# Kernel optimization log

Hardware: AMD Instinct MI355X
Metric: run time of the kernel (lower is better)

Reference implementation:

```python
import jax, jax.numpy as jnp
import numpy as np

HD = 8   # hidden_dim per node
H = 28
W = 28
B = 16


def conv2d(x, w, b):
    y = jax.lax.conv_general_dilated(x, w, (1, 1), 'SAME',
                                     dimension_numbers=('NCHW', 'OIHW', 'NCHW'))
    return y + b[None, :, None, None]


def gru_cell(x, h, td, gw, gb, cw, cb):
    # ConvGRU cell with multiplicative topdown modulation of the gate input.
    combined = jnp.concatenate([x, h], axis=1) * jax.nn.sigmoid(td)  # (B,2HD,H,W)
    r, u = jnp.split(jax.nn.sigmoid(conv2d(combined, gw, gb)), 2, axis=1)
    cand = jnp.tanh(conv2d(jnp.concatenate([x, r * h], axis=1), cw, cb))
    return (1.0 - u) * h + u * cand


def td_proj(td, w, b):
    # dynamic nn.Linear: (B, HD*H*W) -> (B, 2*HD*H*W), reshaped to feature map
    out = td.reshape(td.shape[0], -1) @ w.T + b
    return out.reshape(td.shape[0], 2 * HD, H, W)


def setup_inputs():
    key = jax.random.key(0)
    ks = jax.random.split(key, 16)
    s = 0.02
    return {
        'input_tensor': jax.random.normal(ks[0], (B, 3, 1, H, W), jnp.float32),
        'topdown_input': jax.random.normal(ks[1], (B, 2 * HD, H, W), jnp.float32),
        'input_conv_w': jax.random.normal(ks[2], (HD, 3, 3, 3), jnp.float32) * s,
        'input_conv_b': jnp.zeros((HD,), jnp.float32),
        'gates_w': jax.random.normal(ks[3], (3, 2 * HD, 2 * HD, 3, 3), jnp.float32) * s,
        'gates_b': jnp.zeros((3, 2 * HD), jnp.float32),
        'can_w': jax.random.normal(ks[4], (3, HD, 2 * HD, 3, 3), jnp.float32) * s,
        'can_b': jnp.zeros((3, HD), jnp.float32),
        'td_w0': jax.random.normal(ks[5], (2 * HD * H * W, HD * H * W), jnp.float32) * s,
        'td_b0': jnp.zeros((2 * HD * H * W,), jnp.float32),
        'td_w1': jax.random.normal(ks[6], (2 * HD * H * W, HD * H * W), jnp.float32) * s,
        'td_b1': jnp.zeros((2 * HD * H * W,), jnp.float32),
        'fc1_w': jax.random.normal(ks[7], (100, HD * H * W), jnp.float32) * s,
        'fc1_b': jnp.zeros((100,), jnp.float32),
        'fc2_w': jax.random.normal(ks[8], (10, 100), jnp.float32) * s,
        'fc2_b': jnp.zeros((10,), jnp.float32),
    }


def reference(input_tensor, topdown_input, input_conv_w, input_conv_b,
              gates_w, gates_b, can_w, can_b,
              td_w0, td_b0, td_w1, td_b1, fc1_w, fc1_b, fc2_w, fc2_b):
    b = input_tensor.shape[0]
    z = jnp.zeros((b, HD, H, W), input_tensor.dtype)
    prev = [z, z, z]
    cur = [z, z, z]
    # input layout (b,c,t,h,w); permute+index picks frame t=0
    cur_input = conv2d(input_tensor[:, :, 0], input_conv_w, input_conv_b)
    for step in range(2):  # reps=2, max(seq_len, max_rank)=1 -> 2 graph sweeps
        # node 0 (input node): bottomup = input conv; feedback from node 1 (0.6)
        td0 = td_proj(0.6 * prev[1], td_w0, td_b0)
        cur[0] = gru_cell(cur_input, prev[0], td0,
                          gates_w[0], gates_b[0], can_w[0], can_b[0])
        # node 1: feedforward from node 0 (0.8); feedback from node 2 (0.5)
        td1 = td_proj(0.5 * prev[2], td_w1, td_b1)
        cur[1] = gru_cell(0.8 * prev[0], prev[1], td1,
                          gates_w[1], gates_b[1], can_w[1], can_b[1])
        # node 2 (output node): feedforward from node 1 (0.7); external topdown
        cur[2] = gru_cell(0.7 * prev[1], prev[2], topdown_input,
                          gates_w[2], gates_b[2], can_w[2], can_b[2])
        # faithful to torch: hidden_state_prev = hidden_state_cur aliases the
        # list, so sweeps after the first see in-sweep node updates
        prev = cur
    pred = jax.nn.relu(cur[2].reshape(b, -1)) @ fc1_w.T + fc1_b
    pred = jax.nn.relu(pred) @ fc2_w.T + fc2_b
    return pred
```

## Files before the change

kernel.cpp:

```cpp
#include <hip/hip_runtime.h>
#include <cstddef>

#define HD 8
#define C2 16
#define HH 28
#define WW 28
#define BB 16
#define SP (HH*WW)
#define FEAT (HD*SP)
#define FEAT2 (C2*SP)

#define TILE_ROWS 2
#define NT (HH/TILE_ROWS)
#define NBLK (BB*NT)
#define NTHR 512

#define X0_R 18
#define H00_R 14
#define H10_R 10
#define H11_R 6

__device__ __forceinline__ float sigf(float x) { return 1.0f / (1.0f + expf(-x)); }

union F4 { float4 v; float f[4]; };

struct SM {
    float gwt[C2*9][16];
    float cwt[C2*9][8];
    float gb[C2];
    float cb[HD];
    float hc1[HD];
    float hc2[HD];
    float comb[C2][18][32];
    union {
        float rh[HD][16][32];
        float s_in[3][TILE_ROWS+18][32];
    } u;
    float su[HD][14][32];
    float x0e[HD][X0_R][32];
    float h00e[HD][H00_R][32];
    float h10e[HD][H10_R][32];
    float h11e[HD][H11_R][32];
};

__device__ __forceinline__ void gbar(unsigned* arrive, unsigned* release,
                                     int blk, unsigned ep) {
    __syncthreads();
    __threadfence();
    if (threadIdx.x == 0)
        __hip_atomic_store(&arrive[(size_t)blk * 16], ep,
                           __ATOMIC_RELEASE, __HIP_MEMORY_SCOPE_AGENT);
    if (blk == 0) {
        int t = threadIdx.x;
        if (t < NBLK) {
            while (__hip_atomic_load(&arrive[(size_t)t * 16],
                                     __ATOMIC_RELAXED, __HIP_MEMORY_SCOPE_AGENT) < ep)
                __builtin_amdgcn_s_sleep(32);
        }
        __syncthreads();
        if (t < NBLK)
            __hip_atomic_store(&release[(size_t)t * 16], ep,
                               __ATOMIC_RELEASE, __HIP_MEMORY_SCOPE_AGENT);
    } else {
        if (threadIdx.x == 0) {
            while (__hip_atomic_load(&release[(size_t)blk * 16],
                                     __ATOMIC_RELAXED, __HIP_MEMORY_SCOPE_AGENT) < ep)
                __builtin_amdgcn_s_sleep(32);
        }
    }
    __threadfence();
    __syncthreads();
}

__device__ __forceinline__ void stage_node(SM& sm, int tid, int n,
                           const float* gates_w, const float* gates_b,
                           const float* can_w, const float* can_b) {
    for (int i = tid; i < C2*C2*9; i += NTHR) {
        int oc = i & 15, r = i >> 4;
        sm.gwt[r][oc] = gates_w[n*C2*C2*9 + oc*C2*9 + r];
    }
    for (int i = tid; i < C2*9*8; i += NTHR) {
        int oc = i & 7, r = i >> 3;
        sm.cwt[r][oc] = can_w[n*HD*C2*9 + oc*C2*9 + r];
    }
    if (tid < C2) sm.gb[tid] = gates_b[n*C2 + tid];
    if (tid < HD) sm.cb[tid] = can_b[n*HD + tid];
}

template<int XS>
__device__ __forceinline__ const float* xrow(SM& sm, int c, int ridx) {
    if constexpr (XS == 0) return &sm.x0e[c][ridx][0];
    else if constexpr (XS == 1) return &sm.h10e[c][ridx][0];
    else return &sm.h11e[c][ridx][0];
}

template<int M, int XS, int HS, int OS>
__device__ void cell(SM& sm, int tid, int bi, int r0, float xs,
                     const float* __restrict__ td, float* __restrict__ h12g) {
    constexpr int R1 = M + 4, R2 = M + 2;
    constexpr int NIC = (HS == 0) ? HD : C2;
    const int ca    = (OS == 0) ? r0-6 : (OS == 1) ? r0-4 : (OS == 2) ? r0-2 : r0;
    const int xbase = (XS == 0) ? r0-8 : (XS == 1) ? r0-4 : r0-2;
    const int hbase = r0 - 6;

    for (int i = tid; i < NIC*R1*8; i += NTHR) {
        int ci4 = i & 7, rr = (i >> 3) % R1, c = i / (8*R1);
        int row = ca - 2 + rr;
        F4 v; v.f[0] = v.f[1] = v.f[2] = v.f[3] = 0.0f;
        if (row >= 0 && row < HH) {
            F4 base;
            if (c < HD) {
                base.v = *(const float4*)(xrow<XS>(sm, c, row - xbase) + ci4*4);
                #pragma unroll
                for (int e = 0; e < 4; ++e) base.f[e] *= xs;
            } else {
                if constexpr (HS == 1)
                    base.v = *(const float4*)(&sm.h00e[c-HD][row - hbase][ci4*4]);
                else if constexpr (HS == 2) {
                    float h = sm.hc1[c-HD];
                    base.f[0] = base.f[1] = base.f[2] = base.f[3] = h;
                } else {
                    float h = sm.hc2[c-HD];
                    base.f[0] = base.f[1] = base.f[2] = base.f[3] = h;
                }
            }
            const float* tdr = td + c*SP + row*WW;
            #pragma unroll
            for (int e = 0; e < 4; ++e) {
                int col = ci4*4 + e - 2;
                if (col >= 0 && col < WW)
                    v.f[e] = base.f[e] * sigf(tdr[col]);
            }
        }
        *(float4*)&sm.comb[c][rr][ci4*4] = v.v;
    }
    __syncthreads();

    constexpr int itemsU = 2*M*32;
    if constexpr (HS != 0) {
        constexpr int itemsB = 2*R2*32;
        for (int i = tid; i < itemsB + itemsU; i += NTHR) {
            if (i < itemsB) {
                int ci = i & 31, rr = (i >> 5) % R2, g = i / (32*R2);
                int row = ca - 1 + rr, col = ci - 2;
                bool inb = (col >= 0 && col < WW && row >= 0 && row < HH);
                float a0 = sm.gb[g*4+0], a1 = sm.gb[g*4+1],
                      a2 = sm.gb[g*4+2], a3 = sm.gb[g*4+3];
                if (inb) {
                    #pragma unroll 2
                    for (int ic = 0; ic < C2; ++ic) {
                        const float* wb = &sm.gwt[ic*9][g*4];
                        #pragma unroll
                        for (int dy = 0; dy < 3; ++dy)
                            #pragma unroll
                            for (int dx = 0; dx < 3; ++dx) {
                                float cvv = sm.comb[ic][rr+dy][ci-1+dx];
                                F4 w; w.v = *(const float4*)(wb + (dy*3+dx)*16);
                                a0 += cvv*w.f[0]; a1 += cvv*w.f[1];
                                a2 += cvv*w.f[2]; a3 += cvv*w.f[3];
                            }
                    }
                }
                float av[4] = {a0, a1, a2, a3};
                #pragma unroll
                for (int o = 0; o < 4; ++o) {
                    int c = g*4 + o;
                    float v = 0.0f;
                    if (inb) {
                        float hv;
                        if constexpr (HS == 1) hv = sm.h00e[c][row - hbase][ci];
                        else if constexpr (HS == 2) hv = sm.hc1[c];
                        else hv = sm.hc2[c];
                        v = sigf(av[o]) * hv;
                    }
                    sm.u.rh[c][rr][ci] = v;
                }
            } else {
                int j = i - itemsB;
                int ci = j & 31, rr = (j >> 5) % M, g = j / (32*M);
                int row = ca + rr, col = ci - 2;
                bool inb = (col >= 0 && col < WW && row >= 0 && row < HH);
                float a0 = sm.gb[HD+g*4+0], a1 = sm.gb[HD+g*4+1],
                      a2 = sm.gb[HD+g*4+2], a3 = sm.gb[HD+g*4+3];
                if (inb) {
                    #pragma unroll 2
                    for (int ic = 0; ic < C2; ++ic) {
                        const float* wb = &sm.gwt[ic*9][HD + g*4];
                        #pragma unroll
                        for (int dy = 0; dy < 3; ++dy)
                            #pragma unroll
                            for (int dx = 0; dx < 3; ++dx) {
                                float cvv = sm.comb[ic][rr+1+dy][ci-1+dx];
                                F4 w; w.v = *(const float4*)(wb + (dy*3+dx)*16);
                                a0 += cvv*w.f[0]; a1 += cvv*w.f[1];
                                a2 += cvv*w.f[2]; a3 += cvv*w.f[3];
                            }
                    }
                }
                float av[4] = {a0, a1, a2, a3};
                #pragma unroll
                for (int o = 0; o < 4; ++o)
                    sm.su[g*4+o][rr][ci] = sigf(av[o]);
            }
        }
    } else {
        for (int i = tid; i < itemsU; i += NTHR) {
            int ci = i & 31, rr = (i >> 5) % M, g = i / (32*M);
            int row = ca + rr, col = ci - 2;
            bool inb = (col >= 0 && col < WW && row >= 0 && row < HH);
            float a0 = sm.gb[HD+g*4+0], a1 = sm.gb[HD+g*4+1],
                  a2 = sm.gb[HD+g*4+2], a3 = sm.gb[HD+g*4+3];
            if (inb) {
                #pragma unroll 2
                for (int ic = 0; ic < HD; ++ic) {
                    const float* wb = &sm.gwt[ic*9][HD + g*4];
                    #pragma unroll
                    for (int dy = 0; dy < 3; ++dy)
                        #pragma unroll
                        for (int dx = 0; dx < 3; ++dx) {
                            float cvv = sm.comb[ic][rr+1+dy][ci-1+dx];
                            F4 w; w.v = *(const float4*)(wb + (dy*3+dx)*16);
                            a0 += cvv*w.f[0]; a1 += cvv*w.f[1];
                            a2 += cvv*w.f[2]; a3 += cvv*w.f[3];
                        }
                }
            }
            float av[4] = {a0, a1, a2, a3};
            #pragma unroll
            for (int o = 0; o < 4; ++o)
                sm.su[g*4+o][rr][ci] = sigf(av[o]);
        }
    }
    __syncthreads();

    for (int i = tid; i < 2*M*32; i += NTHR) {
        int ci = i & 31, rr = (i >> 5) % M, g = i / (32*M);
        int row = ca + rr, col = ci - 2;
        bool inb = (col >= 0 && col < WW && row >= 0 && row < HH);
        float a0 = sm.cb[g*4+0], a1 = sm.cb[g*4+1],
              a2 = sm.cb[g*4+2], a3 = sm.cb[g*4+3];
        if (inb) {
            #pragma unroll 2
            for (int ic = 0; ic < HD; ++ic) {
                const float* wb = &sm.cwt[ic*9][g*4];
                #pragma unroll
                for (int dy = 0; dy < 3; ++dy) {
                    const float* xr = xrow<XS>(sm, ic, (row - 1 + dy) - xbase);
                    #pragma unroll
                    for (int dx = 0; dx < 3; ++dx) {
                        float civ = xs * xr[ci-1+dx];
                        F4 w; w.v = *(const float4*)(wb + (dy*3+dx)*8);
                        a0 += civ*w.f[0]; a1 += civ*w.f[1];
                        a2 += civ*w.f[2]; a3 += civ*w.f[3];
                    }
                }
            }
            if constexpr (HS != 0) {
                #pragma unroll 2
                for (int ic = HD; ic < C2; ++ic) {
                    const float* wb = &sm.cwt[ic*9][g*4];
                    #pragma unroll
                    for (int dy = 0; dy < 3; ++dy)
                        #pragma unroll
                        for (int dx = 0; dx < 3; ++dx) {
                            float civ = sm.u.rh[ic-HD][rr+dy][ci-1+dx];
                            F4 w; w.v = *(const float4*)(wb + (dy*3+dx)*8);
                            a0 += civ*w.f[0]; a1 += civ*w.f[1];
                            a2 += civ*w.f[2]; a3 += civ*w.f[3];
                        }
                }
            }
        }
        float av[4] = {a0, a1, a2, a3};
        #pragma unroll
        for (int o = 0; o < 4; ++o) {
            int c = g*4 + o;
            float outv = 0.0f;
            if (inb) {
                float uu = sm.su[c][rr][ci];
                float cand = tanhf(av[o]);
                float hv;
                if constexpr (HS == 1) hv = sm.h00e[c][row - hbase][ci];
                else if constexpr (HS == 2) hv = sm.hc1[c];
                else if constexpr (HS == 3) hv = sm.hc2[c];
                else hv = 0.0f;
                outv = (1.0f - uu) * hv + uu * cand;
            }
            if constexpr (OS == 0) sm.h00e[c][row - (r0-6)][ci] = outv;
            else if constexpr (OS == 1) sm.h10e[c][row - (r0-4)][ci] = outv;
            else if constexpr (OS == 2) sm.h11e[c][row - (r0-2)][ci] = outv;
            else {
                if (inb)
                    h12g[((size_t)bi*HD + c)*SP + row*WW + col] = outv;
            }
        }
    }
    __syncthreads();
}

__global__ void init_kernel(unsigned* arrive, unsigned* release) {
    int t = threadIdx.x;
    for (int i = t; i < NBLK*16; i += 256) { arrive[i] = 0u; release[i] = 0u; }
}

__global__ __launch_bounds__(NTHR, 2)
void mega_kernel(const float* __restrict__ input_tensor, const float* __restrict__ topdown,
                 const float* __restrict__ icw, const float* __restrict__ icb,
                 const float* __restrict__ gates_w, const float* __restrict__ gates_b,
                 const float* __restrict__ can_w, const float* __restrict__ can_b,
                 const float* __restrict__ td_w0, const float* __restrict__ td_b0,
                 const float* __restrict__ td_w1, const float* __restrict__ td_b1,
                 float* __restrict__ h12g,
                 float* __restrict__ td0c, float* __restrict__ td1c,
                 unsigned* arrive, unsigned* release)
{
    const int tid = threadIdx.x;
    const int blk = blockIdx.x;
    const int bi  = blk / NT;
    const int r0  = (blk % NT) * TILE_ROWS;

    __shared__ SM sm;

    if (tid < HD) {
        sm.hc1[tid] = sigf(gates_b[1*C2 + HD + tid]) * tanhf(can_b[1*HD + tid]);
        sm.hc2[tid] = sigf(gates_b[2*C2 + HD + tid]) * tanhf(can_b[2*HD + tid]);
    }
    bool f0 = false, f1 = false;
    for (int c = 0; c < HD; ++c) {
        f0 |= (sigf(gates_b[1*C2 + HD + c]) * tanhf(can_b[1*HD + c])) != 0.0f;
        f1 |= (sigf(gates_b[2*C2 + HD + c]) * tanhf(can_b[2*HD + c])) != 0.0f;
    }

    for (int i = tid; i < 3*(TILE_ROWS+18)*32; i += NTHR) {
        int ci = i & 31, rr = (i >> 5) % (TILE_ROWS+18), c = i / (32*(TILE_ROWS+18));
        int row = r0 - 9 + rr, col = ci - 2;
        float v = 0.0f;
        if (row >= 0 && row < HH && col >= 0 && col < WW)
            v = input_tensor[((size_t)bi*3 + c)*SP + row*WW + col];
        sm.u.s_in[c][rr][ci] = v;
    }
    for (int i = tid; i < 3*9*8; i += NTHR) {
        int oc = i & 7, r = i >> 3;
        sm.gwt[r][oc] = icw[oc*27 + r];
    }
    if (tid < HD) sm.cb[tid] = icb[tid];
    __syncthreads();

    for (int i = tid; i < X0_R*32; i += NTHR) {
        int ci = i & 31, rr = i >> 5;
        int row = r0 - 8 + rr, col = ci - 2;
        float acc[8];
        if (row >= 0 && row < HH && col >= 0 && col < WW) {
            #pragma unroll
            for (int o = 0; o < 8; ++o) acc[o] = sm.cb[o];
            for (int ic = 0; ic < 3; ++ic)
                #pragma unroll
                for (int dy = 0; dy < 3; ++dy)
                    #pragma unroll
                    for (int dx = 0; dx < 3; ++dx) {
                        float a = sm.u.s_in[ic][rr+dy][ci-1+dx];
                        F4 w0, w1;
                        w0.v = *(const float4*)&sm.gwt[ic*9+dy*3+dx][0];
                        w1.v = *(const float4*)&sm.gwt[ic*9+dy*3+dx][4];
                        acc[0] += a*w0.f[0]; acc[1] += a*w0.f[1];
                        acc[2] += a*w0.f[2]; acc[3] += a*w0.f[3];
                        acc[4] += a*w1.f[0]; acc[5] += a*w1.f[1];
                        acc[6] += a*w1.f[2]; acc[7] += a*w1.f[3];
                    }
        } else {
            #pragma unroll
            for (int o = 0; o < 8; ++o) acc[o] = 0.0f;
        }
        #pragma unroll
        for (int o = 0; o < 8; ++o) sm.x0e[o][rr][ci] = acc[o];
    }
    __syncthreads();

    stage_node(sm, tid, 0, gates_w, gates_b, can_w, can_b);
    cell<14, 0, 0, 0>(sm, tid, bi, r0, 1.0f, td_b0, nullptr);

    if (f0 | f1) {
        if (f0) {
            for (int j = blk*NTHR + tid; j < FEAT2; j += NBLK*NTHR) {
                float s = td_b0[j];
                const float* wr = td_w0 + (size_t)j * FEAT;
                for (int c = 0; c < HD; ++c) {
                    float hcv = sm.hc1[c];
                    if (hcv != 0.0f) {
                        float ss = 0.0f;
                        for (int p = 0; p < SP; ++p) ss += wr[c*SP + p];
                        s += 0.6f * hcv * ss;
                    }
                }
                td0c[j] = s;
            }
        }
        if (f1) {
            for (int j = blk*NTHR + tid; j < FEAT2; j += NBLK*NTHR) {
                float s = td_b1[j];
                const float* wr = td_w1 + (size_t)j * FEAT;
                for (int c = 0; c < HD; ++c) {
                    float hcv = sm.hc2[c];
                    if (hcv != 0.0f) {
                        float ss = 0.0f;
                        for (int p = 0; p < SP; ++p) ss += wr[c*SP + p];
                        s += 0.5f * hcv * ss;
                    }
                }
                td1c[j] = s;
            }
        }
        gbar(arrive, release, blk, 1u);
    }
    const float* td0v = f0 ? td0c : td_b0;
    const float* td1v = f1 ? td1c : td_b1;

    cell<10, 0, 1, 1>(sm, tid, bi, r0, 1.0f, td0v, nullptr);

    stage_node(sm, tid, 1, gates_w, gates_b, can_w, can_b);
    cell<6, 1, 2, 2>(sm, tid, bi, r0, 0.8f, td1v, nullptr);

    stage_node(sm, tid, 2, gates_w, gates_b, can_w, can_b);
    cell<2, 2, 3, 3>(sm, tid, bi, r0, 0.7f, topdown + (size_t)bi*FEAT2, h12g);
}

__global__ __launch_bounds__(256)
void fc1_kernel(const float* __restrict__ in, const float* __restrict__ w,
                const float* __restrict__ b, float* __restrict__ out) {
    int j    = blockIdx.x;
    int wave = threadIdx.x >> 6;
    int lane = threadIdx.x & 63;
    float acc[4] = {0.f, 0.f, 0.f, 0.f};
    const float* wr = w + (size_t)j * FEAT;
    for (int k = lane; k < FEAT; k += 64) {
        float wv = wr[k];
        #pragma unroll
        for (int q = 0; q < 4; ++q) {
            float v = in[(size_t)(wave*4+q)*FEAT + k];
            acc[q] += fmaxf(v, 0.0f) * wv;
        }
    }
    #pragma unroll
    for (int off = 32; off > 0; off >>= 1)
        #pragma unroll
        for (int q = 0; q < 4; ++q)
            acc[q] += __shfl_down(acc[q], off);
    if (lane == 0) {
        #pragma unroll
        for (int q = 0; q < 4; ++q)
            out[(size_t)(wave*4+q)*100 + j] = acc[q] + b[j];
    }
}

__global__ __launch_bounds__(256)
void fc2_kernel(const float* __restrict__ p1, const float* __restrict__ w,
                const float* __restrict__ b, float* __restrict__ out) {
    int t = threadIdx.x;
    if (t >= BB*10) return;
    int bi = t / 10, j = t % 10;
    float acc = b[j];
    for (int k = 0; k < 100; ++k)
        acc += fmaxf(p1[bi*100 + k], 0.0f) * w[j*100 + k];
    out[bi*10 + j] = acc;
}

extern "C" void kernel_launch(void* const* d_in, const int* in_sizes, int n_in,
                              void* d_out, int out_size, void* d_ws, size_t ws_size,
                              hipStream_t stream) {
    const float* input_tensor = (const float*)d_in[0];
    const float* topdown      = (const float*)d_in[1];
    const float* icw  = (const float*)d_in[2];
    const float* icb  = (const float*)d_in[3];
    const float* gates_w = (const float*)d_in[4];
    const float* gates_b = (const float*)d_in[5];
    const float* can_w   = (const float*)d_in[6];
    const float* can_b   = (const float*)d_in[7];
    const float* td_w0 = (const float*)d_in[8];
    const float* td_b0 = (const float*)d_in[9];
    const float* td_w1 = (const float*)d_in[10];
    const float* td_b1 = (const float*)d_in[11];
    const float* fc1_w = (const float*)d_in[12];
    const float* fc1_b = (const float*)d_in[13];
    const float* fc2_w = (const float*)d_in[14];
    const float* fc2_b = (const float*)d_in[15];
    float* out = (float*)d_out;

    float* ws   = (float*)d_ws;
    float* h12g = ws;
    float* p1   = h12g + BB*HD*SP;
    float* td0c = p1 + BB*100;
    float* td1c = td0c + FEAT2;
    unsigned* arrive  = (unsigned*)((char*)d_ws + (16u << 20));
    unsigned* release = arrive + NBLK*16;

    init_kernel<<<1, 256, 0, stream>>>(arrive, release);
    mega_kernel<<<NBLK, NTHR, 0, stream>>>(
        input_tensor, topdown, icw, icb, gates_w, gates_b, can_w, can_b,
        td_w0, td_b0, td_w1, td_b1,
        h12g, td0c, td1c, arrive, release);
    fc1_kernel<<<100, 256, 0, stream>>>(h12g, fc1_w, fc1_b, p1);
    fc2_kernel<<<1, 256, 0, stream>>>(p1, fc2_w, fc2_b, out);
}
```

Before: 111.5 us.

## Fuse fc1/fc2 into mega kernel via grid barriers and keep update gate in registers

The fc1 and fc2 layers, which ran as separate kernels, now run at the tail of the persistent mega kernel, separated by two extra grid-wide barriers. This removes two kernel launches and their launch gaps. The update-gate sigmoids are now held in per-thread registers instead of a shared-memory array, which frees LDS and drops one store/load pass, at the cost of extra register pressure and less interleaving of the reset and update convolutions. The spin-wait sleep interval is also halved to cut barrier wake-up latency.

```diff
diff --git a/kernel.cpp b/kernel.cpp
--- a/kernel.cpp
+++ b/kernel.cpp
@@ -36,7 +36,6 @@
         float rh[HD][16][32];
         float s_in[3][TILE_ROWS+18][32];
     } u;
-    float su[HD][14][32];
     float x0e[HD][X0_R][32];
     float h00e[HD][H00_R][32];
     float h10e[HD][H10_R][32];
@@ -55,7 +54,7 @@
         if (t < NBLK) {
             while (__hip_atomic_load(&arrive[(size_t)t * 16],
                                      __ATOMIC_RELAXED, __HIP_MEMORY_SCOPE_AGENT) < ep)
-                __builtin_amdgcn_s_sleep(32);
+                __builtin_amdgcn_s_sleep(16);
         }
         __syncthreads();
         if (t < NBLK)
@@ -65,7 +64,7 @@
         if (threadIdx.x == 0) {
             while (__hip_atomic_load(&release[(size_t)blk * 16],
                                      __ATOMIC_RELAXED, __HIP_MEMORY_SCOPE_AGENT) < ep)
-                __builtin_amdgcn_s_sleep(32);
+                __builtin_amdgcn_s_sleep(16);
         }
     }
     __threadfence();
@@ -99,6 +98,7 @@
                      const float* __restrict__ td, float* __restrict__ h12g) {
     constexpr int R1 = M + 4, R2 = M + 2;
     constexpr int NIC = (HS == 0) ? HD : C2;
+    constexpr int ITER_U = (2*M*32 + NTHR - 1) / NTHR;
     const int ca    = (OS == 0) ? r0-6 : (OS == 1) ? r0-4 : (OS == 2) ? r0-2 : r0;
     const int xbase = (XS == 0) ? r0-8 : (XS == 1) ? r0-4 : r0-2;
     const int hbase = r0 - 6;
@@ -136,75 +136,50 @@
     }
     __syncthreads();
 
-    constexpr int itemsU = 2*M*32;
     if constexpr (HS != 0) {
-        constexpr int itemsB = 2*R2*32;
-        for (int i = tid; i < itemsB + itemsU; i += NTHR) {
-            if (i < itemsB) {
-                int ci = i & 31, rr = (i >> 5) % R2, g = i / (32*R2);
-                int row = ca - 1 + rr, col = ci - 2;
-                bool inb = (col >= 0 && col < WW && row >= 0 && row < HH);
-                float a0 = sm.gb[g*4+0], a1 = sm.gb[g*4+1],
-                      a2 = sm.gb[g*4+2], a3 = sm.gb[g*4+3];
+        for (int i = tid; i < 2*R2*32; i += NTHR) {
+            int ci = i & 31, rr = (i >> 5) % R2, g = i / (32*R2);
+            int row = ca - 1 + rr, col = ci - 2;
+            bool inb = (col >= 0 && col < WW && row >= 0 && row < HH);
+            float a0 = sm.gb[g*4+0], a1 = sm.gb[g*4+1],
+                  a2 = sm.gb[g*4+2], a3 = sm.gb[g*4+3];
+            if (inb) {
+                #pragma unroll 2
+                for (int ic = 0; ic < C2; ++ic) {
+                    const float* wb = &sm.gwt[ic*9][g*4];
+                    #pragma unroll
+                    for (int dy = 0; dy < 3; ++dy)
+                        #pragma unroll
+                        for (int dx = 0; dx < 3; ++dx) {
+                            float cvv = sm.comb[ic][rr+dy][ci-1+dx];
+                            F4 w; w.v = *(const float4*)(wb + (dy*3+dx)*16);
+                            a0 += cvv*w.f[0]; a1 += cvv*w.f[1];
+                            a2 += cvv*w.f[2]; a3 += cvv*w.f[3];
+                        }
+                }
+            }
+            float av[4] = {a0, a1, a2, a3};
+            #pragma unroll
+            for (int o = 0; o < 4; ++o) {
+                int c = g*4 + o;
+                float v = 0.0f;
                 if (inb) {
-                    #pragma unroll 2
-                    for (int ic = 0; ic < C2; ++ic) {
-                        const float* wb = &sm.gwt[ic*9][g*4];
-                        #pragma unroll
-                        for (int dy = 0; dy < 3; ++dy)
-                            #pragma unroll
-                            for (int dx = 0; dx < 3; ++dx) {
-                                float cvv = sm.comb[ic][rr+dy][ci-1+dx];
-                                F4 w; w.v = *(const float4*)(wb + (dy*3+dx)*16);
-                                a0 += cvv*w.f[0]; a1 += cvv*w.f[1];
-                                a2 += cvv*w.f[2]; a3 += cvv*w.f[3];
-                            }
-                    }
-                }
-                float av[4] = {a0, a1, a2, a3};
-                #pragma unroll
-                for (int o = 0; o < 4; ++o) {
-                    int c = g*4 + o;
-                    float v = 0.0f;
-                    if (inb) {
-                        float hv;
-                        if constexpr (HS == 1) hv = sm.h00e[c][row - hbase][ci];
-                        else if constexpr (HS == 2) hv = sm.hc1[c];
-                        else hv = sm.hc2[c];
-                        v = sigf(av[o]) * hv;
-                    }
-                    sm.u.rh[c][rr][ci] = v;
-                }
-            } else {
-                int j = i - itemsB;
-                int ci = j & 31, rr = (j >> 5) % M, g = j / (32*M);
-                int row = ca + rr, col = ci - 2;
-                bool inb = (col >= 0 && col < WW && row >= 0 && row < HH);
-                float a0 = sm.gb[HD+g*4+0], a1 = sm.gb[HD+g*4+1],
-                      a2 = sm.gb[HD+g*4+2], a3 = sm.gb[HD+g*4+3];
-                if (inb) {
-                    #pragma unroll 2
-                    for (int ic = 0; ic < C2; ++ic) {
-                        const float* wb = &sm.gwt[ic*9][HD + g*4];
-                        #pragma unroll
-                        for (int dy = 0; dy < 3; ++dy)
-                            #pragma unroll
-                            for (int dx = 0; dx < 3; ++dx) {
-                                float cvv = sm.comb[ic][rr+1+dy][ci-1+dx];
-                                F4 w; w.v = *(const float4*)(wb + (dy*3+dx)*16);
-                                a0 += cvv*w.f[0]; a1 += cvv*w.f[1];
-                                a2 += cvv*w.f[2]; a3 += cvv*w.f[3];
-                            }
-                    }
-                }
-                float av[4] = {a0, a1, a2, a3};
-                #pragma unroll
-                for (int o = 0; o < 4; ++o)
-                    sm.su[g*4+o][rr][ci] = sigf(av[o]);
-            }
-        }
-    } else {
-        for (int i = tid; i < itemsU; i += NTHR) {
+                    float hv;
+                    if constexpr (HS == 1) hv = sm.h00e[c][row - hbase][ci];
+                    else if constexpr (HS == 2) hv = sm.hc1[c];
+                    else hv = sm.hc2[c];
+                    v = sigf(av[o]) * hv;
+                }
+                sm.u.rh[c][rr][ci] = v;
+            }
+        }
+    }
+
+    float su_reg[ITER_U][4];
+    #pragma unroll
+    for (int k = 0; k < ITER_U; ++k) {
+        int i = tid + k*NTHR;
+        if (i < 2*M*32) {
             int ci = i & 31, rr = (i >> 5) % M, g = i / (32*M);
             int row = ca + rr, col = ci - 2;
             bool inb = (col >= 0 && col < WW && row >= 0 && row < HH);
@@ -212,7 +187,7 @@
                   a2 = sm.gb[HD+g*4+2], a3 = sm.gb[HD+g*4+3];
             if (inb) {
                 #pragma unroll 2
-                for (int ic = 0; ic < HD; ++ic) {
+                for (int ic = 0; ic < NIC; ++ic) {
                     const float* wb = &sm.gwt[ic*9][HD + g*4];
                     #pragma unroll
                     for (int dy = 0; dy < 3; ++dy)
@@ -225,73 +200,75 @@
                         }
                 }
             }
-            float av[4] = {a0, a1, a2, a3};
-            #pragma unroll
-            for (int o = 0; o < 4; ++o)
-                sm.su[g*4+o][rr][ci] = sigf(av[o]);
-        }
-    }
-    __syncthreads();
-
-    for (int i = tid; i < 2*M*32; i += NTHR) {
-        int ci = i & 31, rr = (i >> 5) % M, g = i / (32*M);
-        int row = ca + rr, col = ci - 2;
-        bool inb = (col >= 0 && col < WW && row >= 0 && row < HH);
-        float a0 = sm.cb[g*4+0], a1 = sm.cb[g*4+1],
-              a2 = sm.cb[g*4+2], a3 = sm.cb[g*4+3];
-        if (inb) {
-            #pragma unroll 2
-            for (int ic = 0; ic < HD; ++ic) {
-                const float* wb = &sm.cwt[ic*9][g*4];
-                #pragma unroll
-                for (int dy = 0; dy < 3; ++dy) {
-                    const float* xr = xrow<XS>(sm, ic, (row - 1 + dy) - xbase);
-                    #pragma unroll
-                    for (int dx = 0; dx < 3; ++dx) {
-                        float civ = xs * xr[ci-1+dx];
-                        F4 w; w.v = *(const float4*)(wb + (dy*3+dx)*8);
-                        a0 += civ*w.f[0]; a1 += civ*w.f[1];
-                        a2 += civ*w.f[2]; a3 += civ*w.f[3];
-                    }
-                }
-            }
-            if constexpr (HS != 0) {
+            su_reg[k][0] = sigf(a0); su_reg[k][1] = sigf(a1);
+            su_reg[k][2] = sigf(a2); su_reg[k][3] = sigf(a3);
+        }
+    }
+    __syncthreads();
+
+    #pragma unroll
+    for (int k = 0; k < ITER_U; ++k) {
+        int i = tid + k*NTHR;
+        if (i < 2*M*32) {
+            int ci = i & 31, rr = (i >> 5) % M, g = i / (32*M);
+            int row = ca + rr, col = ci - 2;
+            bool inb = (col >= 0 && col < WW && row >= 0 && row < HH);
+            float a0 = sm.cb[g*4+0], a1 = sm.cb[g*4+1],
+                  a2 = sm.cb[g*4+2], a3 = sm.cb[g*4+3];
+            if (inb) {
                 #pragma unroll 2
-                for (int ic = HD; ic < C2; ++ic) {
+                for (int ic = 0; ic < HD; ++ic) {
                     const float* wb = &sm.cwt[ic*9][g*4];
                     #pragma unroll
-                    for (int dy = 0; dy < 3; ++dy)
+                    for (int dy = 0; dy < 3; ++dy) {
+                        const float* xr = xrow<XS>(sm, ic, (row - 1 + dy) - xbase);
                         #pragma unroll
                         for (int dx = 0; dx < 3; ++dx) {
-                            float civ = sm.u.rh[ic-HD][rr+dy][ci-1+dx];
+                            float civ = xs * xr[ci-1+dx];
                             F4 w; w.v = *(const float4*)(wb + (dy*3+dx)*8);
                             a0 += civ*w.f[0]; a1 += civ*w.f[1];
                             a2 += civ*w.f[2]; a3 += civ*w.f[3];
                         }
-                }
-            }
-        }
-        float av[4] = {a0, a1, a2, a3};
-        #pragma unroll
-        for (int o = 0; o < 4; ++o) {
-            int c = g*4 + o;
-            float outv = 0.0f;
-            if (inb) {
-                float uu = sm.su[c][rr][ci];
-                float cand = tanhf(av[o]);
-                float hv;
-                if constexpr (HS == 1) hv = sm.h00e[c][row - hbase][ci];
-                else if constexpr (HS == 2) hv = sm.hc1[c];
-                else if constexpr (HS == 3) hv = sm.hc2[c];
-                else hv = 0.0f;
-                outv = (1.0f - uu) * hv + uu * cand;
-            }
-            if constexpr (OS == 0) sm.h00e[c][row - (r0-6)][ci] = outv;
-            else if constexpr (OS == 1) sm.h10e[c][row - (r0-4)][ci] = outv;
-            else if constexpr (OS == 2) sm.h11e[c][row - (r0-2)][ci] = outv;
-            else {
-                if (inb)
-                    h12g[((size_t)bi*HD + c)*SP + row*WW + col] = outv;
+                    }
+                }
+                if constexpr (HS != 0) {
+                    #pragma unroll 2
+                    for (int ic = HD; ic < C2; ++ic) {
+                        const float* wb = &sm.cwt[ic*9][g*4];
+                        #pragma unroll
+                        for (int dy = 0; dy < 3; ++dy)
+                            #pragma unroll
+                            for (int dx = 0; dx < 3; ++dx) {
+                                float civ = sm.u.rh[ic-HD][rr+dy][ci-1+dx];
+                                F4 w; w.v = *(const float4*)(wb + (dy*3+dx)*8);
+                                a0 += civ*w.f[0]; a1 += civ*w.f[1];
+                                a2 += civ*w.f[2]; a3 += civ*w.f[3];
+                            }
+                    }
+                }
+            }
+            float av[4] = {a0, a1, a2, a3};
+            #pragma unroll
+            for (int o = 0; o < 4; ++o) {
+                int c = g*4 + o;
+                float outv = 0.0f;
+                if (inb) {
+                    float uu = su_reg[k][o];
+                    float cand = tanhf(av[o]);
+                    float hv;
+                    if constexpr (HS == 1) hv = sm.h00e[c][row - hbase][ci];
+                    else if constexpr (HS == 2) hv = sm.hc1[c];
+                    else if constexpr (HS == 3) hv = sm.hc2[c];
+                    else hv = 0.0f;
+                    outv = (1.0f - uu) * hv + uu * cand;
+                }
+                if constexpr (OS == 0) sm.h00e[c][row - (r0-6)][ci] = outv;
+                else if constexpr (OS == 1) sm.h10e[c][row - (r0-4)][ci] = outv;
+                else if constexpr (OS == 2) sm.h11e[c][row - (r0-2)][ci] = outv;
+                else {
+                    if (inb)
+                        h12g[((size_t)bi*HD + c)*SP + row*WW + col] = outv;
+                }
             }
         }
     }
@@ -310,7 +287,10 @@
                  const float* __restrict__ can_w, const float* __restrict__ can_b,
                  const float* __restrict__ td_w0, const float* __restrict__ td_b0,
                  const float* __restrict__ td_w1, const float* __restrict__ td_b1,
-                 float* __restrict__ h12g,
+                 const float* __restrict__ fc1_w, const float* __restrict__ fc1_b,
+                 const float* __restrict__ fc2_w, const float* __restrict__ fc2_b,
+                 float* __restrict__ out,
+                 float* __restrict__ h12g, float* __restrict__ p1,
                  float* __restrict__ td0c, float* __restrict__ td1c,
                  unsigned* arrive, unsigned* release)
 {
@@ -320,6 +300,7 @@
     const int r0  = (blk % NT) * TILE_ROWS;
 
     __shared__ SM sm;
+    unsigned ep = 0;
 
     if (tid < HD) {
         sm.hc1[tid] = sigf(gates_b[1*C2 + HD + tid]) * tanhf(can_b[1*HD + tid]);
@@ -410,7 +391,7 @@
                 td1c[j] = s;
             }
         }
-        gbar(arrive, release, blk, 1u);
+        gbar(arrive, release, blk, ++ep);
     }
     const float* td0v = f0 ? td0c : td_b0;
     const float* td1v = f1 ? td1c : td_b1;
@@ -422,46 +403,42 @@
 
     stage_node(sm, tid, 2, gates_w, gates_b, can_w, can_b);
     cell<2, 2, 3, 3>(sm, tid, bi, r0, 0.7f, topdown + (size_t)bi*FEAT2, h12g);
-}
-
-__global__ __launch_bounds__(256)
-void fc1_kernel(const float* __restrict__ in, const float* __restrict__ w,
-                const float* __restrict__ b, float* __restrict__ out) {
-    int j    = blockIdx.x;
-    int wave = threadIdx.x >> 6;
-    int lane = threadIdx.x & 63;
-    float acc[4] = {0.f, 0.f, 0.f, 0.f};
-    const float* wr = w + (size_t)j * FEAT;
-    for (int k = lane; k < FEAT; k += 64) {
-        float wv = wr[k];
+
+    gbar(arrive, release, blk, ++ep);
+    if (blk < 100 && tid < 256) {
+        int j    = blk;
+        int wave = tid >> 6;
+        int lane = tid & 63;
+        float acc[4] = {0.f, 0.f, 0.f, 0.f};
+        const float* wr = fc1_w + (size_t)j * FEAT;
+        for (int k = lane; k < FEAT; k += 64) {
+            float wv = wr[k];
+            #pragma unroll
+            for (int q = 0; q < 4; ++q) {
+                float v = h12g[(size_t)(wave*4+q)*FEAT + k];
+                acc[q] += fmaxf(v, 0.0f) * wv;
+            }
+        }
         #pragma unroll
-        for (int q = 0; q < 4; ++q) {
-            float v = in[(size_t)(wave*4+q)*FEAT + k];
-            acc[q] += fmaxf(v, 0.0f) * wv;
-        }
-    }
-    #pragma unroll
-    for (int off = 32; off > 0; off >>= 1)
-        #pragma unroll
-        for (int q = 0; q < 4; ++q)
-            acc[q] += __shfl_down(acc[q], off);
-    if (lane == 0) {
-        #pragma unroll
-        for (int q = 0; q < 4; ++q)
-            out[(size_t)(wave*4+q)*100 + j] = acc[q] + b[j];
-    }
-}
-
-__global__ __launch_bounds__(256)
-void fc2_kernel(const float* __restrict__ p1, const float* __restrict__ w,
-                const float* __restrict__ b, float* __restrict__ out) {
-    int t = threadIdx.x;
-    if (t >= BB*10) return;
-    int bi = t / 10, j = t % 10;
-    float acc = b[j];
-    for (int k = 0; k < 100; ++k)
-        acc += fmaxf(p1[bi*100 + k], 0.0f) * w[j*100 + k];
-    out[bi*10 + j] = acc;
+        for (int off = 32; off > 0; off >>= 1)
+            #pragma unroll
+            for (int q = 0; q < 4; ++q)
+                acc[q] += __shfl_down(acc[q], off);
+        if (lane == 0) {
+            #pragma unroll
+            for (int q = 0; q < 4; ++q)
+                p1[(size_t)(wave*4+q)*100 + j] = acc[q] + fc1_b[j];
+        }
+    }
+
+    gbar(arrive, release, blk, ++ep);
+    if (blk == 0 && tid < BB*10) {
+        int b2 = tid / 10, j = tid % 10;
+        float acc = fc2_b[j];
+        for (int k = 0; k < 100; ++k)
+            acc += fmaxf(p1[b2*100 + k], 0.0f) * fc2_w[j*100 + k];
+        out[b2*10 + j] = acc;
+    }
 }
 
 extern "C" void kernel_launch(void* const* d_in, const int* in_sizes, int n_in,
@@ -496,8 +473,6 @@
     init_kernel<<<1, 256, 0, stream>>>(arrive, release);
     mega_kernel<<<NBLK, NTHR, 0, stream>>>(
         input_tensor, topdown, icw, icb, gates_w, gates_b, can_w, can_b,
-        td_w0, td_b0, td_w1, td_b1,
-        h12g, td0c, td1c, arrive, release);
-    fc1_kernel<<<100, 256, 0, stream>>>(h12g, fc1_w, fc1_b, p1);
-    fc2_kernel<<<1, 256, 0, stream>>>(p1, fc2_w, fc2_b, out);
-}
+        td_w0, td_b0, td_w1, td_b1, fc1_w, fc1_b, fc2_w, fc2_b, out,
+        h12g, p1, td0c, td1c, arrive, release);
+}
```

After: 201.6 us. 80.8% more time.
